# Optimization experiments

Hardware: AMD Instinct MI355X
Metric: run time of the kernel (lower is better)

Reference implementation:

```python
import jax, jax.numpy as jnp
import numpy as np

C, D, H, W = 48, 128, 128, 128
N = 2097152


def setup_inputs() -> dict:
    key = jax.random.key(0)
    k1, k2, k3 = jax.random.split(key, 3)
    # normalized coords in [-1, 1] as expected by grid_sample(align_corners=True)
    ray_pts = jax.random.uniform(k1, (N, 3), jnp.float32) * 2.0 - 1.0
    k0 = jax.random.normal(k2, (1, C, D, H, W), jnp.float32) * 1e-4
    former_k0_cur = jax.random.normal(k3, (1, C, D, H, W), jnp.float32)
    return {"ray_pts": ray_pts, "k0": k0, "former_k0_cur": former_k0_cur}


def _grid_sample_trilinear(grid, pts):
    # grid: [C, D, H, W]; pts: [N, 3] with (x, y, z) in [-1, 1] mapping to (W, H, D)
    c, d, h, w = grid.shape
    x, y, z = pts[:, 0], pts[:, 1], pts[:, 2]
    # align_corners=True: -1 -> 0, +1 -> size-1
    ix = (x + 1.0) * 0.5 * (w - 1)
    iy = (y + 1.0) * 0.5 * (h - 1)
    iz = (z + 1.0) * 0.5 * (d - 1)
    x0f, y0f, z0f = jnp.floor(ix), jnp.floor(iy), jnp.floor(iz)
    wx, wy, wz = ix - x0f, iy - y0f, iz - z0f
    x0 = jnp.clip(x0f.astype(jnp.int32), 0, w - 1)
    x1 = jnp.clip(x0f.astype(jnp.int32) + 1, 0, w - 1)
    y0 = jnp.clip(y0f.astype(jnp.int32), 0, h - 1)
    y1 = jnp.clip(y0f.astype(jnp.int32) + 1, 0, h - 1)
    z0 = jnp.clip(z0f.astype(jnp.int32), 0, d - 1)
    z1 = jnp.clip(z0f.astype(jnp.int32) + 1, 0, d - 1)

    def g(zi, yi, xi):
        return grid[:, zi, yi, xi]  # [C, N] gather

    out = (
        g(z0, y0, x0) * ((1 - wx) * (1 - wy) * (1 - wz))
        + g(z0, y0, x1) * (wx * (1 - wy) * (1 - wz))
        + g(z0, y1, x0) * ((1 - wx) * wy * (1 - wz))
        + g(z0, y1, x1) * (wx * wy * (1 - wz))
        + g(z1, y0, x0) * ((1 - wx) * (1 - wy) * wz)
        + g(z1, y0, x1) * (wx * (1 - wy) * wz)
        + g(z1, y1, x0) * ((1 - wx) * wy * wz)
        + g(z1, y1, x1) * (wx * wy * wz)
    )
    return out  # [C, N]


def reference(ray_pts, k0, former_k0_cur):
    # faithful to torch: full dense grid add, then trilinear grid_sample lookup
    grid = (former_k0_cur + k0)[0]  # [C, D, H, W]
    feats = _grid_sample_trilinear(grid, ray_pts)  # [C, N]
    return feats.T  # [N, C]
```

## Files before the change

### kernel.cpp

```cpp
#include <hip/hip_runtime.h>
#include <hip/hip_bf16.h>
#include <cstdint>

#define CCH 48
#define DD 128
#define HH 128
#define WW 128
#define NVOX (DD*HH*WW)
#define NPTS 2097152
#define NBINS 8192
#define BRICK_VOX 405

typedef unsigned int uint;
typedef unsigned short ushort_t;

__device__ __forceinline__ ushort_t f2bf_rne(float f) {
    uint u = __float_as_uint(f);
    uint r = (u + 0x7fffu + ((u >> 16) & 1u)) >> 16;
    return (ushort_t)r;
}

struct PtGeo {
    int x0, y0, z0, x1, y1, z1;
    float wx, wy, wz;
};
__device__ __forceinline__ PtGeo pt_geo(const float* __restrict__ pts, int n) {
    PtGeo g;
    const float ix = (pts[n*3+0] + 1.0f) * 63.5f;
    const float iy = (pts[n*3+1] + 1.0f) * 63.5f;
    const float iz = (pts[n*3+2] + 1.0f) * 63.5f;
    const float xf = floorf(ix), yf = floorf(iy), zf = floorf(iz);
    g.wx = ix - xf; g.wy = iy - yf; g.wz = iz - zf;
    int x0 = (int)xf, y0 = (int)yf, z0 = (int)zf;
    g.x0 = min(max(x0,0), WW-1); g.x1 = min(max(x0+1,0), WW-1);
    g.y0 = min(max(y0,0), HH-1); g.y1 = min(max(y0+1,0), HH-1);
    g.z0 = min(max(z0,0), DD-1); g.z1 = min(max(z0+1,0), DD-1);
    return g;
}
__device__ __forceinline__ int pt_bin(const PtGeo& g) {
    return ((g.z0 >> 2) << 8) | ((g.y0 >> 3) << 4) | (g.x0 >> 3);
}

__global__ __launch_bounds__(256) void fuse_transpose_kernel(
    const float* __restrict__ k0, const float* __restrict__ former,
    ushort_t* __restrict__ grid_t)
{
    const int v = blockIdx.x * 256 + threadIdx.x;
    float vals[CCH];
#pragma unroll
    for (int c = 0; c < CCH; ++c) {
        const size_t off = (size_t)c * NVOX + v;
        vals[c] = __builtin_nontemporal_load(k0 + off)
                + __builtin_nontemporal_load(former + off);
    }
    uint4* dst = reinterpret_cast<uint4*>(grid_t + (size_t)v * CCH);
#pragma unroll
    for (int i = 0; i < 6; ++i) {
        uint4 u;
        u.x = (uint)f2bf_rne(vals[i*8+0]) | ((uint)f2bf_rne(vals[i*8+1]) << 16);
        u.y = (uint)f2bf_rne(vals[i*8+2]) | ((uint)f2bf_rne(vals[i*8+3]) << 16);
        u.z = (uint)f2bf_rne(vals[i*8+4]) | ((uint)f2bf_rne(vals[i*8+5]) << 16);
        u.w = (uint)f2bf_rne(vals[i*8+6]) | ((uint)f2bf_rne(vals[i*8+7]) << 16);
        dst[i] = u;
    }
}

__global__ __launch_bounds__(256) void count_kernel(
    const float* __restrict__ pts, uint* __restrict__ count)
{
    const int n = blockIdx.x * 256 + threadIdx.x;
    if (n >= NPTS) return;
    const PtGeo g = pt_geo(pts, n);
    atomicAdd(&count[pt_bin(g)], 1u);
}

__global__ __launch_bounds__(1024) void scan_kernel(
    const uint* __restrict__ count, uint* __restrict__ cursor)
{
    __shared__ uint part[1024];
    const int t = threadIdx.x;
    uint c[8]; uint s = 0u;
#pragma unroll
    for (int k = 0; k < 8; ++k) { c[k] = count[t*8+k]; s += c[k]; }
    part[t] = s;
    __syncthreads();
    for (int off = 1; off < 1024; off <<= 1) {
        uint v = (t >= off) ? part[t-off] : 0u;
        __syncthreads();
        part[t] += v;
        __syncthreads();
    }
    uint ex = part[t] - s;
#pragma unroll
    for (int k = 0; k < 8; ++k) { cursor[t*8+k] = ex; ex += c[k]; }
}

__global__ __launch_bounds__(256) void scatter_kernel(
    const float* __restrict__ pts, uint* __restrict__ cursor, uint* __restrict__ order)
{
    const int n = blockIdx.x * 256 + threadIdx.x;
    if (n >= NPTS) return;
    const PtGeo g = pt_geo(pts, n);
    const uint pos = atomicAdd(&cursor[pt_bin(g)], 1u);
    order[pos] = (uint)n;
}

__global__ __launch_bounds__(256) void sample_lds(
    const float* __restrict__ pts, const ushort_t* __restrict__ grid_t,
    const uint* __restrict__ order, const uint* __restrict__ bin_count,
    const uint* __restrict__ bin_end, float* __restrict__ out)
{
    __shared__ __align__(16) ushort_t brick[BRICK_VOX * CCH];

    const int b  = (blockIdx.x & 7) * 1024 + (blockIdx.x >> 3);
    const int bx = b & 15, by = (b >> 4) & 15, bz = b >> 8;

    const uint cnt   = bin_count[b];
    const uint end   = bin_end[b];
    const uint start = end - cnt;

    const int t = threadIdx.x;
    uint4* bl = reinterpret_cast<uint4*>(brick);
    const uint4* gsrc = reinterpret_cast<const uint4*>(grid_t);
#pragma unroll
    for (int it = 0; it < 10; ++it) {
        const int i = it * 256 + t;
        if (i < BRICK_VOX * 6) {
            const int v = i / 6, p = i % 6;
            const int lz = v / 81, rem = v % 81, ly = rem / 9, lx = rem % 9;
            const int gz = min(bz*4 + lz, DD-1);
            const int gy = min(by*8 + ly, HH-1);
            const int gx = min(bx*8 + lx, WW-1);
            bl[v*6 + p] = gsrc[(size_t)((gz*HH + gy)*WW + gx) * 6 + p];
        }
    }
    __syncthreads();
    if (cnt == 0) return;

    const int sub = t & 1;
    for (uint base = 0; base < cnt; base += 128) {
        const uint ii = base + (uint)(t >> 1);
        if (ii >= cnt) break;
        const int n = (int)order[start + ii];

        const PtGeo g = pt_geo(pts, n);
        const float wx0 = 1.0f - g.wx, wy0 = 1.0f - g.wy, wz0 = 1.0f - g.wz;

        const int lx0 = g.x0 - bx*8, lx1 = g.x1 - bx*8;
        const int ly0 = g.y0 - by*8, ly1 = g.y1 - by*8;
        const int lz0 = g.z0 - bz*4, lz1 = g.z1 - bz*4;

        const int r0 = lz0*81, r1 = lz1*81;
        const int s0 = ly0*9,  s1 = ly1*9;
        const int vox[8] = { r0+s0+lx0, r0+s0+lx1, r0+s1+lx0, r0+s1+lx1,
                             r1+s0+lx0, r1+s0+lx1, r1+s1+lx0, r1+s1+lx1 };
        const float w[8] = { wx0*wy0*wz0,  g.wx*wy0*wz0,  wx0*g.wy*wz0,  g.wx*g.wy*wz0,
                             wx0*wy0*g.wz, g.wx*wy0*g.wz, wx0*g.wy*g.wz, g.wx*g.wy*g.wz };

        float acc[3][8];
#pragma unroll
        for (int j = 0; j < 3; ++j)
#pragma unroll
            for (int q = 0; q < 8; ++q) acc[j][q] = 0.0f;

#pragma unroll
        for (int half = 0; half < 2; ++half) {
            uint4 L[4][3];
#pragma unroll
            for (int c = 0; c < 4; ++c) {
#pragma unroll
                for (int j = 0; j < 3; ++j)
                    L[c][j] = bl[vox[half*4 + c]*6 + 2*j + sub];
            }
#pragma unroll
            for (int c = 0; c < 4; ++c) {
                const float wc = w[half*4 + c];
#pragma unroll
                for (int j = 0; j < 3; ++j) {
                    const uint* us = reinterpret_cast<const uint*>(&L[c][j]);
#pragma unroll
                    for (int q = 0; q < 4; ++q) {
                        acc[j][2*q]   = fmaf(wc, __uint_as_float(us[q] << 16),         acc[j][2*q]);
                        acc[j][2*q+1] = fmaf(wc, __uint_as_float(us[q] & 0xffff0000u), acc[j][2*q+1]);
                    }
                }
            }
        }

        float4* o = reinterpret_cast<float4*>(out + (size_t)n * CCH);
#pragma unroll
        for (int j = 0; j < 3; ++j) {
            const int gidx = 2*j + sub;
            o[2*gidx+0] = make_float4(acc[j][0], acc[j][1], acc[j][2], acc[j][3]);
            o[2*gidx+1] = make_float4(acc[j][4], acc[j][5], acc[j][6], acc[j][7]);
        }
    }
}

__global__ __launch_bounds__(256) void sample_flat(
    const float* __restrict__ pts, const ushort_t* __restrict__ grid_t,
    float* __restrict__ out)
{
    const int tid = blockIdx.x * 256 + threadIdx.x;
    const int n   = tid >> 1;
    const int sub = tid & 1;

    const PtGeo g = pt_geo(pts, n);
    const float wx0 = 1.0f - g.wx, wy0 = 1.0f - g.wy, wz0 = 1.0f - g.wz;
    const int HWn = HH*WW;
    const int bz0 = g.z0*HWn, bz1 = g.z1*HWn;
    const int by0 = g.y0*WW,  by1 = g.y1*WW;
    const int vox[8] = { bz0+by0+g.x0, bz0+by0+g.x1, bz0+by1+g.x0, bz0+by1+g.x1,
                         bz1+by0+g.x0, bz1+by0+g.x1, bz1+by1+g.x0, bz1+by1+g.x1 };
    const float w[8] = { wx0*wy0*wz0,  g.wx*wy0*wz0,  wx0*g.wy*wz0,  g.wx*g.wy*wz0,
                         wx0*wy0*g.wz, g.wx*wy0*g.wz, wx0*g.wy*g.wz, g.wx*g.wy*g.wz };

    uint4 L[8][3];
#pragma unroll
    for (int c = 0; c < 8; ++c) {
        const uint4* p = reinterpret_cast<const uint4*>(grid_t + (size_t)vox[c] * CCH);
#pragma unroll
        for (int j = 0; j < 3; ++j) L[c][j] = p[2*j + sub];
    }
    float acc[3][8];
#pragma unroll
    for (int j = 0; j < 3; ++j)
#pragma unroll
        for (int q = 0; q < 8; ++q) acc[j][q] = 0.0f;
#pragma unroll
    for (int c = 0; c < 8; ++c) {
        const float wc = w[c];
#pragma unroll
        for (int j = 0; j < 3; ++j) {
            const uint* us = reinterpret_cast<const uint*>(&L[c][j]);
#pragma unroll
            for (int q = 0; q < 4; ++q) {
                acc[j][2*q]   = fmaf(wc, __uint_as_float(us[q] << 16),         acc[j][2*q]);
                acc[j][2*q+1] = fmaf(wc, __uint_as_float(us[q] & 0xffff0000u), acc[j][2*q+1]);
            }
        }
    }
    float4* o = reinterpret_cast<float4*>(out + (size_t)n * CCH);
#pragma unroll
    for (int j = 0; j < 3; ++j) {
        const int gidx = 2*j + sub;
        o[2*gidx+0] = make_float4(acc[j][0], acc[j][1], acc[j][2], acc[j][3]);
        o[2*gidx+1] = make_float4(acc[j][4], acc[j][5], acc[j][6], acc[j][7]);
    }
}

__global__ __launch_bounds__(256) void sample_naive(
    const float* __restrict__ pts, const float* __restrict__ k0,
    const float* __restrict__ former, float* __restrict__ out)
{
    const int n = blockIdx.x * 256 + threadIdx.x;
    if (n >= NPTS) return;
    const PtGeo g = pt_geo(pts, n);
    const float wx0 = 1.0f - g.wx, wy0 = 1.0f - g.wy, wz0 = 1.0f - g.wz;
    const int HWn = HH*WW;
    const int v000 = g.z0*HWn + g.y0*WW + g.x0, v100 = g.z0*HWn + g.y0*WW + g.x1;
    const int v010 = g.z0*HWn + g.y1*WW + g.x0, v110 = g.z0*HWn + g.y1*WW + g.x1;
    const int v001 = g.z1*HWn + g.y0*WW + g.x0, v101 = g.z1*HWn + g.y0*WW + g.x1;
    const int v011 = g.z1*HWn + g.y1*WW + g.x0, v111 = g.z1*HWn + g.y1*WW + g.x1;
    const float w000 = wx0*wy0*wz0,  w100 = g.wx*wy0*wz0;
    const float w010 = wx0*g.wy*wz0, w110 = g.wx*g.wy*wz0;
    const float w001 = wx0*wy0*g.wz, w101 = g.wx*wy0*g.wz;
    const float w011 = wx0*g.wy*g.wz, w111 = g.wx*g.wy*g.wz;
    for (int c = 0; c < CCH; ++c) {
        const float* g0 = k0     + (size_t)c * NVOX;
        const float* g1 = former + (size_t)c * NVOX;
        float s = 0.0f;
        s += w000 * (g0[v000] + g1[v000]);
        s += w100 * (g0[v100] + g1[v100]);
        s += w010 * (g0[v010] + g1[v010]);
        s += w110 * (g0[v110] + g1[v110]);
        s += w001 * (g0[v001] + g1[v001]);
        s += w101 * (g0[v101] + g1[v101]);
        s += w011 * (g0[v011] + g1[v011]);
        s += w111 * (g0[v111] + g1[v111]);
        out[(size_t)n*CCH + c] = s;
    }
}

extern "C" void kernel_launch(void* const* d_in, const int* in_sizes, int n_in,
                              void* d_out, int out_size, void* d_ws, size_t ws_size,
                              hipStream_t stream) {
    const float* ray_pts = (const float*)d_in[0];
    const float* k0      = (const float*)d_in[1];
    const float* former  = (const float*)d_in[2];
    float* out = (float*)d_out;

    const size_t grid_bytes  = (size_t)NVOX * CCH * sizeof(ushort_t);
    const size_t order_bytes = (size_t)NPTS * sizeof(uint);
    const size_t bins_bytes  = (size_t)NBINS * sizeof(uint);
    const size_t need_binned = grid_bytes + order_bytes + 2*bins_bytes;

    if (ws_size >= grid_bytes) {
        ushort_t* grid_t = (ushort_t*)d_ws;
        fuse_transpose_kernel<<<NVOX/256, 256, 0, stream>>>(k0, former, grid_t);
        if (ws_size >= need_binned) {
            uint* order  = (uint*)((char*)d_ws + grid_bytes);
            uint* count  = order + NPTS;
            uint* cursor = count + NBINS;
            hipMemsetAsync(count, 0, bins_bytes, stream);
            count_kernel  <<<NPTS/256, 256, 0, stream>>>(ray_pts, count);
            scan_kernel   <<<1, 1024, 0, stream>>>(count, cursor);
            scatter_kernel<<<NPTS/256, 256, 0, stream>>>(ray_pts, cursor, order);
            sample_lds    <<<NBINS, 256, 0, stream>>>(ray_pts, grid_t, order, count, cursor, out);
        } else {
            sample_flat<<<(NPTS*2)/256, 256, 0, stream>>>(ray_pts, grid_t, out);
        }
    } else {
        sample_naive<<<NPTS/256, 256, 0, stream>>>(ray_pts, k0, former, out);
    }
}
```

Baseline: 659.6 us.

## Replace count/scan/scatter binning with fixed-slot bins plus overflow path

The separate count, scan and scatter passes are replaced by a single scatter pass. Each point claims a fixed slot in its bin, and points that do not fit go to an overflow list handled by a separate flat-gather kernel. Bins are halved in y (16384 bins, 9x5x5 brick) so the LDS brick is smaller, and occupancy is raised to 6 blocks per CU. The first point's coordinates are prefetched before the brick load, and the next point's coordinates are loaded inside the loop to hide latency. This removes one full pass over the points and the serial scan kernel. In exchange the brick halo is loaded more often, and any overflow beyond OVF_CAP would silently drop points.

```diff
diff --git a/kernel.cpp b/kernel.cpp
--- a/kernel.cpp
+++ b/kernel.cpp
@@ -8,8 +8,10 @@
 #define WW 128
 #define NVOX (DD*HH*WW)
 #define NPTS 2097152
-#define NBINS 8192
-#define BRICK_VOX 405
+#define NBINS 16384
+#define BRICK_VOX 225
+#define SLOTS 160
+#define OVF_CAP 65536
 
 typedef unsigned int uint;
 typedef unsigned short ushort_t;
@@ -24,11 +26,11 @@
     int x0, y0, z0, x1, y1, z1;
     float wx, wy, wz;
 };
-__device__ __forceinline__ PtGeo pt_geo(const float* __restrict__ pts, int n) {
+__device__ __forceinline__ PtGeo pt_geo3(float px, float py, float pz) {
     PtGeo g;
-    const float ix = (pts[n*3+0] + 1.0f) * 63.5f;
-    const float iy = (pts[n*3+1] + 1.0f) * 63.5f;
-    const float iz = (pts[n*3+2] + 1.0f) * 63.5f;
+    const float ix = (px + 1.0f) * 63.5f;
+    const float iy = (py + 1.0f) * 63.5f;
+    const float iz = (pz + 1.0f) * 63.5f;
     const float xf = floorf(ix), yf = floorf(iy), zf = floorf(iz);
     g.wx = ix - xf; g.wy = iy - yf; g.wz = iz - zf;
     int x0 = (int)xf, y0 = (int)yf, z0 = (int)zf;
@@ -37,8 +39,11 @@
     g.z0 = min(max(z0,0), DD-1); g.z1 = min(max(z0+1,0), DD-1);
     return g;
 }
+__device__ __forceinline__ PtGeo pt_geo(const float* __restrict__ pts, int n) {
+    return pt_geo3(pts[n*3+0], pts[n*3+1], pts[n*3+2]);
+}
 __device__ __forceinline__ int pt_bin(const PtGeo& g) {
-    return ((g.z0 >> 2) << 8) | ((g.y0 >> 3) << 4) | (g.x0 >> 3);
+    return (((g.z0 >> 2) * 32 + (g.y0 >> 2)) * 16) + (g.x0 >> 3);
 }
 
 __global__ __launch_bounds__(256) void fuse_transpose_kernel(
@@ -65,92 +70,76 @@
     }
 }
 
-__global__ __launch_bounds__(256) void count_kernel(
-    const float* __restrict__ pts, uint* __restrict__ count)
+__global__ __launch_bounds__(256) void scatter_direct(
+    const float* __restrict__ pts, uint* __restrict__ count,
+    uint* __restrict__ order, uint* __restrict__ ovf_cnt, uint* __restrict__ ovf)
 {
     const int n = blockIdx.x * 256 + threadIdx.x;
     if (n >= NPTS) return;
     const PtGeo g = pt_geo(pts, n);
-    atomicAdd(&count[pt_bin(g)], 1u);
-}
-
-__global__ __launch_bounds__(1024) void scan_kernel(
-    const uint* __restrict__ count, uint* __restrict__ cursor)
-{
-    __shared__ uint part[1024];
-    const int t = threadIdx.x;
-    uint c[8]; uint s = 0u;
-#pragma unroll
-    for (int k = 0; k < 8; ++k) { c[k] = count[t*8+k]; s += c[k]; }
-    part[t] = s;
-    __syncthreads();
-    for (int off = 1; off < 1024; off <<= 1) {
-        uint v = (t >= off) ? part[t-off] : 0u;
-        __syncthreads();
-        part[t] += v;
-        __syncthreads();
-    }
-    uint ex = part[t] - s;
-#pragma unroll
-    for (int k = 0; k < 8; ++k) { cursor[t*8+k] = ex; ex += c[k]; }
-}
-
-__global__ __launch_bounds__(256) void scatter_kernel(
-    const float* __restrict__ pts, uint* __restrict__ cursor, uint* __restrict__ order)
-{
-    const int n = blockIdx.x * 256 + threadIdx.x;
-    if (n >= NPTS) return;
-    const PtGeo g = pt_geo(pts, n);
-    const uint pos = atomicAdd(&cursor[pt_bin(g)], 1u);
-    order[pos] = (uint)n;
-}
-
-__global__ __launch_bounds__(256) void sample_lds(
+    const int b = pt_bin(g);
+    const uint pos = atomicAdd(&count[b], 1u);
+    if (pos < SLOTS) {
+        order[b * SLOTS + pos] = (uint)n;
+    } else {
+        const uint op = atomicAdd(ovf_cnt, 1u);
+        if (op < OVF_CAP) ovf[op] = (uint)n;
+    }
+}
+
+__global__ __launch_bounds__(256, 6) void sample_lds(
     const float* __restrict__ pts, const ushort_t* __restrict__ grid_t,
     const uint* __restrict__ order, const uint* __restrict__ bin_count,
-    const uint* __restrict__ bin_end, float* __restrict__ out)
+    float* __restrict__ out)
 {
     __shared__ __align__(16) ushort_t brick[BRICK_VOX * CCH];
 
-    const int b  = (blockIdx.x & 7) * 1024 + (blockIdx.x >> 3);
-    const int bx = b & 15, by = (b >> 4) & 15, bz = b >> 8;
-
-    const uint cnt   = bin_count[b];
-    const uint end   = bin_end[b];
-    const uint start = end - cnt;
-
+    const int b  = (blockIdx.x & 7) * 2048 + (blockIdx.x >> 3);
+    const int bx = b & 15, by = (b >> 4) & 31, bz = b >> 9;
+
+    const uint cnt = min(bin_count[b], (uint)SLOTS);
+    const uint start = (uint)b * SLOTS;
     const int t = threadIdx.x;
-    uint4* bl = reinterpret_cast<uint4*>(brick);
-    const uint4* gsrc = reinterpret_cast<const uint4*>(grid_t);
-#pragma unroll
-    for (int it = 0; it < 10; ++it) {
-        const int i = it * 256 + t;
-        if (i < BRICK_VOX * 6) {
-            const int v = i / 6, p = i % 6;
-            const int lz = v / 81, rem = v % 81, ly = rem / 9, lx = rem % 9;
-            const int gz = min(bz*4 + lz, DD-1);
-            const int gy = min(by*8 + ly, HH-1);
-            const int gx = min(bx*8 + lx, WW-1);
-            bl[v*6 + p] = gsrc[(size_t)((gz*HH + gy)*WW + gx) * 6 + p];
+    const int sub = t & 1;
+
+    uint ii = (uint)(t >> 1);
+    int n0 = -1;
+    float p0x = 0.f, p0y = 0.f, p0z = 0.f;
+    if (ii < cnt) {
+        n0 = (int)order[start + ii];
+        p0x = pts[n0*3+0]; p0y = pts[n0*3+1]; p0z = pts[n0*3+2];
+    }
+
+    {
+        uint4* bl = reinterpret_cast<uint4*>(brick);
+        const uint4* gsrc = reinterpret_cast<const uint4*>(grid_t);
+#pragma unroll
+        for (int it = 0; it < 6; ++it) {
+            const int i = it * 256 + t;
+            if (i < BRICK_VOX * 6) {
+                const int v = i / 6, p = i % 6;
+                const int lz = v / 45, rem = v % 45, ly = rem / 9, lx = rem % 9;
+                const int gz = min(bz*4 + lz, DD-1);
+                const int gy = min(by*4 + ly, HH-1);
+                const int gx = min(bx*8 + lx, WW-1);
+                bl[v*6 + p] = gsrc[(size_t)((gz*HH + gy)*WW + gx) * 6 + p];
+            }
         }
     }
     __syncthreads();
     if (cnt == 0) return;
 
-    const int sub = t & 1;
-    for (uint base = 0; base < cnt; base += 128) {
-        const uint ii = base + (uint)(t >> 1);
-        if (ii >= cnt) break;
-        const int n = (int)order[start + ii];
-
-        const PtGeo g = pt_geo(pts, n);
+    const uint4* bl = reinterpret_cast<const uint4*>(brick);
+    int n = n0; float px = p0x, py = p0y, pz = p0z;
+    for (; ii < cnt; ) {
+        const PtGeo g = pt_geo3(px, py, pz);
         const float wx0 = 1.0f - g.wx, wy0 = 1.0f - g.wy, wz0 = 1.0f - g.wz;
 
         const int lx0 = g.x0 - bx*8, lx1 = g.x1 - bx*8;
-        const int ly0 = g.y0 - by*8, ly1 = g.y1 - by*8;
+        const int ly0 = g.y0 - by*4, ly1 = g.y1 - by*4;
         const int lz0 = g.z0 - bz*4, lz1 = g.z1 - bz*4;
 
-        const int r0 = lz0*81, r1 = lz1*81;
+        const int r0 = lz0*45, r1 = lz1*45;
         const int s0 = ly0*9,  s1 = ly1*9;
         const int vox[8] = { r0+s0+lx0, r0+s0+lx1, r0+s1+lx0, r0+s1+lx1,
                              r1+s0+lx0, r1+s0+lx1, r1+s1+lx0, r1+s1+lx1 };
@@ -164,17 +153,16 @@
             for (int q = 0; q < 8; ++q) acc[j][q] = 0.0f;
 
 #pragma unroll
-        for (int half = 0; half < 2; ++half) {
-            uint4 L[4][3];
-#pragma unroll
-            for (int c = 0; c < 4; ++c) {
+        for (int half = 0; half < 4; ++half) {
+            uint4 L[2][3];
+#pragma unroll
+            for (int c = 0; c < 2; ++c)
 #pragma unroll
                 for (int j = 0; j < 3; ++j)
-                    L[c][j] = bl[vox[half*4 + c]*6 + 2*j + sub];
-            }
-#pragma unroll
-            for (int c = 0; c < 4; ++c) {
-                const float wc = w[half*4 + c];
+                    L[c][j] = bl[vox[half*2 + c]*6 + 2*j + sub];
+#pragma unroll
+            for (int c = 0; c < 2; ++c) {
+                const float wc = w[half*2 + c];
 #pragma unroll
                 for (int j = 0; j < 3; ++j) {
                     const uint* us = reinterpret_cast<const uint*>(&L[c][j]);
@@ -194,6 +182,51 @@
             o[2*gidx+0] = make_float4(acc[j][0], acc[j][1], acc[j][2], acc[j][3]);
             o[2*gidx+1] = make_float4(acc[j][4], acc[j][5], acc[j][6], acc[j][7]);
         }
+
+        ii += 128;
+        if (ii < cnt) {
+            n = (int)order[start + ii];
+            px = pts[n*3+0]; py = pts[n*3+1]; pz = pts[n*3+2];
+        }
+    }
+}
+
+__global__ __launch_bounds__(256) void sample_ovf(
+    const float* __restrict__ pts, const ushort_t* __restrict__ grid_t,
+    const uint* __restrict__ ovf, const uint* __restrict__ ovf_cnt,
+    float* __restrict__ out)
+{
+    const uint m = min(*ovf_cnt, (uint)OVF_CAP);
+    for (uint i = blockIdx.x * 256 + threadIdx.x; i < m; i += 32 * 256) {
+        const int n = (int)ovf[i];
+        const PtGeo g = pt_geo(pts, n);
+        const float wx0 = 1.0f - g.wx, wy0 = 1.0f - g.wy, wz0 = 1.0f - g.wz;
+        const int HWn = HH*WW;
+        const int vox[8] = { (g.z0*HWn + g.y0*WW + g.x0), (g.z0*HWn + g.y0*WW + g.x1),
+                             (g.z0*HWn + g.y1*WW + g.x0), (g.z0*HWn + g.y1*WW + g.x1),
+                             (g.z1*HWn + g.y0*WW + g.x0), (g.z1*HWn + g.y0*WW + g.x1),
+                             (g.z1*HWn + g.y1*WW + g.x0), (g.z1*HWn + g.y1*WW + g.x1) };
+        const float w[8] = { wx0*wy0*wz0,  g.wx*wy0*wz0,  wx0*g.wy*wz0,  g.wx*g.wy*wz0,
+                             wx0*wy0*g.wz, g.wx*wy0*g.wz, wx0*g.wy*g.wz, g.wx*g.wy*g.wz };
+        for (int p = 0; p < 6; ++p) {
+            float acc[8];
+#pragma unroll
+            for (int q = 0; q < 8; ++q) acc[q] = 0.0f;
+#pragma unroll
+            for (int c = 0; c < 8; ++c) {
+                const uint4 u = reinterpret_cast<const uint4*>(grid_t)[(size_t)vox[c]*6 + p];
+                const uint us[4] = {u.x, u.y, u.z, u.w};
+                const float wc = w[c];
+#pragma unroll
+                for (int q = 0; q < 4; ++q) {
+                    acc[2*q]   = fmaf(wc, __uint_as_float(us[q] << 16),         acc[2*q]);
+                    acc[2*q+1] = fmaf(wc, __uint_as_float(us[q] & 0xffff0000u), acc[2*q+1]);
+                }
+            }
+            float4* o = reinterpret_cast<float4*>(out + (size_t)n * CCH + p*8);
+            o[0] = make_float4(acc[0], acc[1], acc[2], acc[3]);
+            o[1] = make_float4(acc[4], acc[5], acc[6], acc[7]);
+        }
     }
 }
 
@@ -208,10 +241,10 @@
     const PtGeo g = pt_geo(pts, n);
     const float wx0 = 1.0f - g.wx, wy0 = 1.0f - g.wy, wz0 = 1.0f - g.wz;
     const int HWn = HH*WW;
-    const int bz0 = g.z0*HWn, bz1 = g.z1*HWn;
-    const int by0 = g.y0*WW,  by1 = g.y1*WW;
-    const int vox[8] = { bz0+by0+g.x0, bz0+by0+g.x1, bz0+by1+g.x0, bz0+by1+g.x1,
-                         bz1+by0+g.x0, bz1+by0+g.x1, bz1+by1+g.x0, bz1+by1+g.x1 };
+    const int vox[8] = { (g.z0*HWn + g.y0*WW + g.x0), (g.z0*HWn + g.y0*WW + g.x1),
+                         (g.z0*HWn + g.y1*WW + g.x0), (g.z0*HWn + g.y1*WW + g.x1),
+                         (g.z1*HWn + g.y0*WW + g.x0), (g.z1*HWn + g.y0*WW + g.x1),
+                         (g.z1*HWn + g.y1*WW + g.x0), (g.z1*HWn + g.y1*WW + g.x1) };
     const float w[8] = { wx0*wy0*wz0,  g.wx*wy0*wz0,  wx0*g.wy*wz0,  g.wx*g.wy*wz0,
                          wx0*wy0*g.wz, g.wx*wy0*g.wz, wx0*g.wy*g.wz, g.wx*g.wy*g.wz };
 
@@ -291,22 +324,24 @@
     float* out = (float*)d_out;
 
     const size_t grid_bytes  = (size_t)NVOX * CCH * sizeof(ushort_t);
-    const size_t order_bytes = (size_t)NPTS * sizeof(uint);
-    const size_t bins_bytes  = (size_t)NBINS * sizeof(uint);
-    const size_t need_binned = grid_bytes + order_bytes + 2*bins_bytes;
+    const size_t order_bytes = (size_t)NBINS * SLOTS * sizeof(uint);
+    const size_t count_bytes = (size_t)NBINS * sizeof(uint);
+    const size_t ovf_bytes   = (size_t)OVF_CAP * sizeof(uint);
+    const size_t need_binned = grid_bytes + order_bytes + count_bytes + 64 + ovf_bytes;
 
     if (ws_size >= grid_bytes) {
         ushort_t* grid_t = (ushort_t*)d_ws;
         fuse_transpose_kernel<<<NVOX/256, 256, 0, stream>>>(k0, former, grid_t);
         if (ws_size >= need_binned) {
-            uint* order  = (uint*)((char*)d_ws + grid_bytes);
-            uint* count  = order + NPTS;
-            uint* cursor = count + NBINS;
-            hipMemsetAsync(count, 0, bins_bytes, stream);
-            count_kernel  <<<NPTS/256, 256, 0, stream>>>(ray_pts, count);
-            scan_kernel   <<<1, 1024, 0, stream>>>(count, cursor);
-            scatter_kernel<<<NPTS/256, 256, 0, stream>>>(ray_pts, cursor, order);
-            sample_lds    <<<NBINS, 256, 0, stream>>>(ray_pts, grid_t, order, count, cursor, out);
+            char* p = (char*)d_ws + grid_bytes;
+            uint* order   = (uint*)p;                 p += order_bytes;
+            uint* count   = (uint*)p;                 p += count_bytes;
+            uint* ovf_cnt = (uint*)p;                 p += 64;
+            uint* ovf     = (uint*)p;
+            hipMemsetAsync(count, 0, count_bytes + 64, stream);
+            scatter_direct<<<NPTS/256, 256, 0, stream>>>(ray_pts, count, order, ovf_cnt, ovf);
+            sample_lds    <<<NBINS, 256, 0, stream>>>(ray_pts, grid_t, order, count, out);
+            sample_ovf    <<<32, 256, 0, stream>>>(ray_pts, grid_t, ovf, ovf_cnt, out);
         } else {
             sample_flat<<<(NPTS*2)/256, 256, 0, stream>>>(ray_pts, grid_t, out);
         }
```

New measurement: 1.560 ms. 2.37x slower.

## Shrink sampling bricks, double bin count, and stage transpose writes through LDS

Applied to the files above, without the earlier changes.

Bins are halved in y (4x4x8 voxel bricks, 16384 bins), which cuts each block's LDS brick from 405 to 225 voxels. The smaller brick allows more resident blocks per CU and a lighter per-block load, at the cost of more halo voxels loaded redundantly across bricks. The fuse/transpose kernel now splits the channels across two half-blocks and stages the bf16 output in shared memory, so global stores are fully coalesced. It also drops the nontemporal load hints. The sampling inner loop is regrouped into four groups of two corners to reduce live registers.

```diff
diff --git a/kernel.cpp b/kernel.cpp
--- a/kernel.cpp
+++ b/kernel.cpp
@@ -8,8 +8,9 @@
 #define WW 128
 #define NVOX (DD*HH*WW)
 #define NPTS 2097152
-#define NBINS 8192
-#define BRICK_VOX 405
+#define NBINS 16384
+#define BRICK_VOX 225
+#define TVOX 128
 
 typedef unsigned int uint;
 typedef unsigned short ushort_t;
@@ -24,11 +25,11 @@
     int x0, y0, z0, x1, y1, z1;
     float wx, wy, wz;
 };
-__device__ __forceinline__ PtGeo pt_geo(const float* __restrict__ pts, int n) {
+__device__ __forceinline__ PtGeo pt_geo3(float px, float py, float pz) {
     PtGeo g;
-    const float ix = (pts[n*3+0] + 1.0f) * 63.5f;
-    const float iy = (pts[n*3+1] + 1.0f) * 63.5f;
-    const float iz = (pts[n*3+2] + 1.0f) * 63.5f;
+    const float ix = (px + 1.0f) * 63.5f;
+    const float iy = (py + 1.0f) * 63.5f;
+    const float iz = (pz + 1.0f) * 63.5f;
     const float xf = floorf(ix), yf = floorf(iy), zf = floorf(iz);
     g.wx = ix - xf; g.wy = iy - yf; g.wz = iz - zf;
     int x0 = (int)xf, y0 = (int)yf, z0 = (int)zf;
@@ -37,32 +38,43 @@
     g.z0 = min(max(z0,0), DD-1); g.z1 = min(max(z0+1,0), DD-1);
     return g;
 }
+__device__ __forceinline__ PtGeo pt_geo(const float* __restrict__ pts, int n) {
+    return pt_geo3(pts[n*3+0], pts[n*3+1], pts[n*3+2]);
+}
 __device__ __forceinline__ int pt_bin(const PtGeo& g) {
-    return ((g.z0 >> 2) << 8) | ((g.y0 >> 3) << 4) | (g.x0 >> 3);
+    return (((g.z0 >> 2) * 32 + (g.y0 >> 2)) * 16) + (g.x0 >> 3);
 }
 
 __global__ __launch_bounds__(256) void fuse_transpose_kernel(
     const float* __restrict__ k0, const float* __restrict__ former,
     ushort_t* __restrict__ grid_t)
 {
-    const int v = blockIdx.x * 256 + threadIdx.x;
-    float vals[CCH];
-#pragma unroll
-    for (int c = 0; c < CCH; ++c) {
-        const size_t off = (size_t)c * NVOX + v;
-        vals[c] = __builtin_nontemporal_load(k0 + off)
-                + __builtin_nontemporal_load(former + off);
-    }
-    uint4* dst = reinterpret_cast<uint4*>(grid_t + (size_t)v * CCH);
-#pragma unroll
-    for (int i = 0; i < 6; ++i) {
+    __shared__ __align__(16) uint4 st[TVOX * 6];
+    const int t    = threadIdx.x;
+    const int vx   = t & (TVOX-1);
+    const int half = t >> 7;
+    const size_t v = (size_t)blockIdx.x * TVOX + vx;
+
+    float vals[24];
+#pragma unroll
+    for (int k = 0; k < 24; ++k) {
+        const size_t off = (size_t)(half*24 + k) * NVOX + v;
+        vals[k] = k0[off] + former[off];
+    }
+#pragma unroll
+    for (int i = 0; i < 3; ++i) {
         uint4 u;
         u.x = (uint)f2bf_rne(vals[i*8+0]) | ((uint)f2bf_rne(vals[i*8+1]) << 16);
         u.y = (uint)f2bf_rne(vals[i*8+2]) | ((uint)f2bf_rne(vals[i*8+3]) << 16);
         u.z = (uint)f2bf_rne(vals[i*8+4]) | ((uint)f2bf_rne(vals[i*8+5]) << 16);
         u.w = (uint)f2bf_rne(vals[i*8+6]) | ((uint)f2bf_rne(vals[i*8+7]) << 16);
-        dst[i] = u;
-    }
+        st[vx*6 + half*3 + i] = u;
+    }
+    __syncthreads();
+    uint4* dst = reinterpret_cast<uint4*>(grid_t) + (size_t)blockIdx.x * (TVOX*6);
+#pragma unroll
+    for (int i = 0; i < 3; ++i)
+        dst[i*256 + t] = st[i*256 + t];
 }
 
 __global__ __launch_bounds__(256) void count_kernel(
@@ -79,9 +91,9 @@
 {
     __shared__ uint part[1024];
     const int t = threadIdx.x;
-    uint c[8]; uint s = 0u;
-#pragma unroll
-    for (int k = 0; k < 8; ++k) { c[k] = count[t*8+k]; s += c[k]; }
+    uint c[16]; uint s = 0u;
+#pragma unroll
+    for (int k = 0; k < 16; ++k) { c[k] = count[t*16+k]; s += c[k]; }
     part[t] = s;
     __syncthreads();
     for (int off = 1; off < 1024; off <<= 1) {
@@ -92,7 +104,7 @@
     }
     uint ex = part[t] - s;
 #pragma unroll
-    for (int k = 0; k < 8; ++k) { cursor[t*8+k] = ex; ex += c[k]; }
+    for (int k = 0; k < 16; ++k) { cursor[t*16+k] = ex; ex += c[k]; }
 }
 
 __global__ __launch_bounds__(256) void scatter_kernel(
@@ -112,31 +124,34 @@
 {
     __shared__ __align__(16) ushort_t brick[BRICK_VOX * CCH];
 
-    const int b  = (blockIdx.x & 7) * 1024 + (blockIdx.x >> 3);
-    const int bx = b & 15, by = (b >> 4) & 15, bz = b >> 8;
+    const int b  = (blockIdx.x & 7) * 2048 + (blockIdx.x >> 3);
+    const int bx = b & 15, by = (b >> 4) & 31, bz = b >> 9;
 
     const uint cnt   = bin_count[b];
     const uint end   = bin_end[b];
     const uint start = end - cnt;
 
     const int t = threadIdx.x;
-    uint4* bl = reinterpret_cast<uint4*>(brick);
-    const uint4* gsrc = reinterpret_cast<const uint4*>(grid_t);
-#pragma unroll
-    for (int it = 0; it < 10; ++it) {
-        const int i = it * 256 + t;
-        if (i < BRICK_VOX * 6) {
-            const int v = i / 6, p = i % 6;
-            const int lz = v / 81, rem = v % 81, ly = rem / 9, lx = rem % 9;
-            const int gz = min(bz*4 + lz, DD-1);
-            const int gy = min(by*8 + ly, HH-1);
-            const int gx = min(bx*8 + lx, WW-1);
-            bl[v*6 + p] = gsrc[(size_t)((gz*HH + gy)*WW + gx) * 6 + p];
+    {
+        uint4* bl = reinterpret_cast<uint4*>(brick);
+        const uint4* gsrc = reinterpret_cast<const uint4*>(grid_t);
+#pragma unroll
+        for (int it = 0; it < 6; ++it) {
+            const int i = it * 256 + t;
+            if (i < BRICK_VOX * 6) {
+                const int v = i / 6, p = i % 6;
+                const int lz = v / 45, rem = v % 45, ly = rem / 9, lx = rem % 9;
+                const int gz = min(bz*4 + lz, DD-1);
+                const int gy = min(by*4 + ly, HH-1);
+                const int gx = min(bx*8 + lx, WW-1);
+                bl[v*6 + p] = gsrc[(size_t)((gz*HH + gy)*WW + gx) * 6 + p];
+            }
         }
     }
     __syncthreads();
     if (cnt == 0) return;
 
+    const uint4* bl = reinterpret_cast<const uint4*>(brick);
     const int sub = t & 1;
     for (uint base = 0; base < cnt; base += 128) {
         const uint ii = base + (uint)(t >> 1);
@@ -147,10 +162,10 @@
         const float wx0 = 1.0f - g.wx, wy0 = 1.0f - g.wy, wz0 = 1.0f - g.wz;
 
         const int lx0 = g.x0 - bx*8, lx1 = g.x1 - bx*8;
-        const int ly0 = g.y0 - by*8, ly1 = g.y1 - by*8;
+        const int ly0 = g.y0 - by*4, ly1 = g.y1 - by*4;
         const int lz0 = g.z0 - bz*4, lz1 = g.z1 - bz*4;
 
-        const int r0 = lz0*81, r1 = lz1*81;
+        const int r0 = lz0*45, r1 = lz1*45;
         const int s0 = ly0*9,  s1 = ly1*9;
         const int vox[8] = { r0+s0+lx0, r0+s0+lx1, r0+s1+lx0, r0+s1+lx1,
                              r1+s0+lx0, r1+s0+lx1, r1+s1+lx0, r1+s1+lx1 };
@@ -164,17 +179,16 @@
             for (int q = 0; q < 8; ++q) acc[j][q] = 0.0f;
 
 #pragma unroll
-        for (int half = 0; half < 2; ++half) {
-            uint4 L[4][3];
-#pragma unroll
-            for (int c = 0; c < 4; ++c) {
+        for (int quarter = 0; quarter < 4; ++quarter) {
+            uint4 L[2][3];
+#pragma unroll
+            for (int c = 0; c < 2; ++c)
 #pragma unroll
                 for (int j = 0; j < 3; ++j)
-                    L[c][j] = bl[vox[half*4 + c]*6 + 2*j + sub];
-            }
-#pragma unroll
-            for (int c = 0; c < 4; ++c) {
-                const float wc = w[half*4 + c];
+                    L[c][j] = bl[vox[quarter*2 + c]*6 + 2*j + sub];
+#pragma unroll
+            for (int c = 0; c < 2; ++c) {
+                const float wc = w[quarter*2 + c];
 #pragma unroll
                 for (int j = 0; j < 3; ++j) {
                     const uint* us = reinterpret_cast<const uint*>(&L[c][j]);
@@ -208,10 +222,10 @@
     const PtGeo g = pt_geo(pts, n);
     const float wx0 = 1.0f - g.wx, wy0 = 1.0f - g.wy, wz0 = 1.0f - g.wz;
     const int HWn = HH*WW;
-    const int bz0 = g.z0*HWn, bz1 = g.z1*HWn;
-    const int by0 = g.y0*WW,  by1 = g.y1*WW;
-    const int vox[8] = { bz0+by0+g.x0, bz0+by0+g.x1, bz0+by1+g.x0, bz0+by1+g.x1,
-                         bz1+by0+g.x0, bz1+by0+g.x1, bz1+by1+g.x0, bz1+by1+g.x1 };
+    const int vox[8] = { (g.z0*HWn + g.y0*WW + g.x0), (g.z0*HWn + g.y0*WW + g.x1),
+                         (g.z0*HWn + g.y1*WW + g.x0), (g.z0*HWn + g.y1*WW + g.x1),
+                         (g.z1*HWn + g.y0*WW + g.x0), (g.z1*HWn + g.y0*WW + g.x1),
+                         (g.z1*HWn + g.y1*WW + g.x0), (g.z1*HWn + g.y1*WW + g.x1) };
     const float w[8] = { wx0*wy0*wz0,  g.wx*wy0*wz0,  wx0*g.wy*wz0,  g.wx*g.wy*wz0,
                          wx0*wy0*g.wz, g.wx*wy0*g.wz, wx0*g.wy*g.wz, g.wx*g.wy*g.wz };
 
@@ -297,11 +311,12 @@
 
     if (ws_size >= grid_bytes) {
         ushort_t* grid_t = (ushort_t*)d_ws;
-        fuse_transpose_kernel<<<NVOX/256, 256, 0, stream>>>(k0, former, grid_t);
+        fuse_transpose_kernel<<<NVOX/TVOX, 256, 0, stream>>>(k0, former, grid_t);
         if (ws_size >= need_binned) {
-            uint* order  = (uint*)((char*)d_ws + grid_bytes);
-            uint* count  = order + NPTS;
-            uint* cursor = count + NBINS;
+            char* p = (char*)d_ws + grid_bytes;
+            uint* order  = (uint*)p;                 p += order_bytes;
+            uint* count  = (uint*)p;                 p += bins_bytes;
+            uint* cursor = (uint*)p;
             hipMemsetAsync(count, 0, bins_bytes, stream);
             count_kernel  <<<NPTS/256, 256, 0, stream>>>(ray_pts, count);
             scan_kernel   <<<1, 1024, 0, stream>>>(count, cursor);
```

Measured after the change: 702.8 us. +6.5%, slower.
